# Kernel optimization log

Measured on AMD Instinct MI355X. Metric: run time of the kernel, lower is better.

## Reference

```python
import jax, jax.numpy as jnp
from jax import lax
import numpy as np

NEG = -1e10  # matches the -10000000000.0 boundary in the torch code


def _nw_forward(theta, A):
    """Needleman-Wunsch DP with softmax (logsumexp) smoothed max.

    V[i, j] = theta[i-1, j-1] + LSE(A + V[i-1, j], V[i-1, j-1], A + V[i, j-1])
    with V[0, 0] = 0 and V[i, 0] = V[0, j] = -1e10 otherwise.
    Vectorized over anti-diagonals (wavefront): diag d holds V[i, d-i].
    """
    N, M = theta.shape
    i_idx = jnp.arange(N + 1)

    # diag d=0: only V[0,0]=0 is on it; diag d=1: V[0,1]=V[1,0]=NEG
    d0 = jnp.full((N + 1,), NEG, dtype=theta.dtype).at[0].set(0.0)
    d1 = jnp.full((N + 1,), NEG, dtype=theta.dtype)

    def step(carry, d):
        pprev, prev = carry  # diagonals d-2 and d-1, indexed by i
        j = d - i_idx
        valid = (i_idx >= 1) & (j >= 1) & (j <= M)
        pad = jnp.full((1,), NEG, dtype=theta.dtype)
        up = jnp.concatenate([pad, prev[:-1]])     # V[i-1, j]   (diag d-1, idx i-1)
        diag = jnp.concatenate([pad, pprev[:-1]])  # V[i-1, j-1] (diag d-2, idx i-1)
        left = prev                                # V[i, j-1]   (diag d-1, idx i)
        ic = jnp.clip(i_idx - 1, 0, N - 1)
        jc = jnp.clip(j - 1, 0, M - 1)
        th = jnp.where(valid, theta[ic, jc], 0.0)
        # candidates in original order (x, m, y)
        cand = jnp.stack([A + up, diag, A + left], axis=-1)  # (N+1, 3)
        v = th + jax.nn.logsumexp(cand, axis=-1)
        new = jnp.where(valid, v, NEG)
        return (prev, new), None

    ds = jnp.arange(2, N + M + 1)
    (_, last), _ = lax.scan(step, (d0, d1), ds)
    return last[N]  # V[N, M] lives on diagonal d = N + M at index i = N


def setup_inputs() -> dict:
    key = jax.random.key(0)
    N, M = 2048, 2048
    theta = jax.random.normal(key, (N, M), dtype=jnp.float32)
    A = jnp.asarray(-4.0, dtype=jnp.float32)  # scalar gap penalty
    return {"theta": theta, "A": A}


def reference(theta, A):
    return _nw_forward(theta, A)
```

## Files before the change

kernel.cpp:

```cpp
#include <hip/hip_runtime.h>


constexpr int NDP = 2048;
constexpr int MDP = 2048;
constexpr int G    = 16;
constexpr int RPW  = 128;
constexpr int BATCH = 32;
constexpr int NB    = 68;
constexpr int DTOT  = NDP + MDP;
constexpr int DVB   = 4224;
constexpr float LOG2E = 1.44269504088896340736f;
constexpr float LN2   = 0.69314718055994530942f;

__device__ __forceinline__ float neginf() { return __int_as_float(0xff800000); }

__device__ __forceinline__ void ic_store(float* p, float v) {
  asm volatile("global_store_dword %0, %1, off sc0 sc1" :: "v"(p), "v"(v));
}
__device__ __forceinline__ void ic_store_flag(int* p, int v) {
  asm volatile("s_waitcnt vmcnt(0)\n\tglobal_store_dword %0, %1, off sc0 sc1"
               :: "v"(p), "v"(v));
}
__device__ __forceinline__ float ic_load(const float* p) {
  float r;
  asm volatile("global_load_dword %0, %1, off sc0 sc1\n\ts_waitcnt vmcnt(0)"
               : "=v"(r) : "v"(p));
  return r;
}
__device__ __forceinline__ int ic_load_flag(const int* p) {
  int r;
  asm volatile("global_load_dword %0, %1, off sc0 sc1\n\ts_waitcnt vmcnt(0)"
               : "=v"(r) : "v"(p) : "memory");
  return r;
}

__global__ __launch_bounds__(64)
void nw_pipe(const float* __restrict__ theta, const float* __restrict__ Aptr,
             float* __restrict__ out, float* __restrict__ vbBase,
             int* __restrict__ flags)
{
  const int wg   = blockIdx.x;
  const int lane = threadIdx.x;

  const float A  = Aptr[0];
  const float eA = __builtin_exp2f(A * LOG2E);

  const int S   = wg * RPW + 2;
  const int rA0 = wg * RPW + 2 * lane;
  const int rB0 = rA0 + 1;
  const float* thA_p = theta + (size_t)rA0 * MDP;
  const float* thB_p = theta + (size_t)rB0 * MDP;
  const int endA = rA0 + 1 + MDP;
  const int endB = endA + 1;

  float* vbMine = vbBase + (size_t)wg * DVB;
  const float* vbProd = vbBase + (size_t)(wg - 1) * DVB;
  int* flagProd = flags + (wg - 1) * 16;
  int* flagMine = flags + wg * 16;
  const int eMaxProd = (wg > 0) ? (wg * RPW + MDP) : -1;

  float WA1 = 0.f, WA2 = 0.f, WB1 = 0.f;
  float upPrev = 0.f;
  float bu = 0.f, bd = (wg == 0) ? 1.f : 0.f;
  float oaccF = 0.f;
  bool  init  = (wg == 0);
  float corner = 0.f;
  float vbReg = neginf();

  float tba[4][8], tbb[4][8];
#pragma unroll
  for (int u = 0; u < 4; ++u)
#pragma unroll
    for (int k = 0; k < 8; ++k) {
      int d  = S + 8 * u + k;
      int cA = min(max(d - (rA0 + 1) - 1, 0), MDP - 1);
      int cB = min(max(d - (rB0 + 1) - 1, 0), MDP - 1);
      tba[u][k] = thA_p[cA];
      tbb[u][k] = thB_p[cB];
    }

  if (wg > 0) {
    const int E0 = S - 1;
    const int need = min(E0 + 31, eMaxProd);
    while (ic_load_flag(flagProd) < need) __builtin_amdgcn_s_sleep(1);
    int e  = E0 + (lane & 31);
    int eL = min(max(e, 0), eMaxProd);
    float v0 = ic_load(vbProd + eL);
    vbReg = (e <= eMaxProd) ? v0 : neginf();
    float m = vbReg;
#pragma unroll
    for (int sh = 1; sh < 64; sh <<= 1) m = fmaxf(m, __shfl_xor(m, sh, 64));
    if (m > -1e30f) { oaccF = m; init = true; }
    bu = __builtin_exp2f(fminf(__shfl(vbReg, 0, 64) - oaccF, 120.f));
  }

  for (int b = 0; b < NB; ++b) {
    const int dBase = S + BATCH * b;
#pragma unroll
    for (int u = 0; u < 4; ++u) {
#pragma unroll
      for (int k = 0; k < 8; ++k) {
        const int d = dBase + 8 * u + k;
        float upA = __shfl_up(WB1, 1, 64);
        if (lane == 0) upA = bu;
        float dgA = (lane == 0) ? bd : upPrev;
        const float tA = __builtin_exp2f(tba[u][k] * LOG2E);
        const float tB = __builtin_exp2f(tbb[u][k] * LOG2E);
        float nA = tA * (eA * (upA + WA1) + dgA);
        float nB = tB * (eA * (WA1 + WB1) + WA2);
        nA = (d <= endA) ? nA : 0.f;
        nB = (d <= endB) ? nB : 0.f;
        WA2 = WA1; WA1 = nA; WB1 = nB; upPrev = upA;
        if (lane == 63) {
          float vlog = __builtin_log2f(WB1) + oaccF;
          ic_store(vbMine + d, vlog);
          if (d == DTOT) corner = vlog;
        }
        bd = bu;
        if (!(u == 3 && k == 7)) {
          float v = __shfl(vbReg, 8 * u + k + 1, 64);
          bu = __builtin_exp2f(fminf(v - oaccF, 120.f));
        }
      }
      {
        float m = fmaxf(fmaxf(WA1, WB1), fmaxf(WA2, upPrev));
        m = fmaxf(m, fmaxf(bu, bd));
#pragma unroll
        for (int sh = 1; sh < 64; sh <<= 1) m = fmaxf(m, __shfl_xor(m, sh, 64));
        int e = 0;
        if (m > 0.f) e = (int)((__float_as_uint(m) >> 23) & 0xFFu) - 126;
        if (e != 0) {
          WA1 = ldexpf(WA1, -e); WA2 = ldexpf(WA2, -e); WB1 = ldexpf(WB1, -e);
          upPrev = ldexpf(upPrev, -e);
          bu = ldexpf(bu, -e); bd = ldexpf(bd, -e);
          oaccF += (float)e;
        }
      }
      if (b + 1 < NB) {
#pragma unroll
        for (int k = 0; k < 8; ++k) {
          int d  = dBase + BATCH + 8 * u + k;
          int cA = min(max(d - (rA0 + 1) - 1, 0), MDP - 1);
          int cB = min(max(d - (rB0 + 1) - 1, 0), MDP - 1);
          tba[u][k] = thA_p[cA];
          tbb[u][k] = thB_p[cB];
        }
      }
    }
    if (wg < G - 1 && lane == 63)
      ic_store_flag(flagMine, dBase + BATCH - 1);
    if (b + 1 < NB && wg > 0) {
      const int E0 = S - 1 + BATCH * (b + 1);
      if (E0 <= eMaxProd) {
        const int need = min(E0 + 31, eMaxProd);
        while (ic_load_flag(flagProd) < need) __builtin_amdgcn_s_sleep(1);
        int e  = E0 + (lane & 31);
        int eL = min(max(e, 0), eMaxProd);
        float v0 = ic_load(vbProd + eL);
        vbReg = (e <= eMaxProd) ? v0 : neginf();
      } else {
        vbReg = neginf();
      }
      if (!init) {
        float m = vbReg;
#pragma unroll
        for (int sh = 1; sh < 64; sh <<= 1) m = fmaxf(m, __shfl_xor(m, sh, 64));
        if (m > -1e30f) { oaccF = m; init = true; }
      }
      bu = __builtin_exp2f(fminf(__shfl(vbReg, 0, 64) - oaccF, 120.f));
    }
  }

  if (wg == G - 1 && lane == 63) out[0] = corner * LN2;
}

constexpr int NTH = 512;
constexpr int RPT = 4;
constexpr int NWAVE = NTH / 64;

__global__ __launch_bounds__(NTH)
void nw_single(const float* __restrict__ th, const float* __restrict__ Aptr,
               float* __restrict__ out)
{
  const int tid  = threadIdx.x;
  const int lane = tid & 63;
  const int wid  = tid >> 6;
  __shared__ float handW[2][NTH];
  __shared__ float wmax[2][NWAVE];
  const float A  = Aptr[0];
  const float eA = __builtin_exp2f(A * LOG2E);
  const int i_base = tid * RPT + 1;
  float W10=0.f,W11=0.f,W12=0.f,W13=0.f,W20=0.f,W21=0.f,W22=0.f,W23=0.f;
  float nb1 = 0.f, nb2 = (tid == 0) ? 1.f : 0.f;
  int oacc = 0;
  const float* thb = th + (size_t)(i_base - 1) * MDP;
  auto loadTh = [&](int d) -> float4 {
    float4 r;
    int c0 = min(max(d - i_base - 1, 0), MDP - 1);
    int c1 = min(max(d - i_base - 2, 0), MDP - 1);
    int c2 = min(max(d - i_base - 3, 0), MDP - 1);
    int c3 = min(max(d - i_base - 4, 0), MDP - 1);
    r.x = thb[c0]; r.y = thb[(size_t)MDP + c1];
    r.z = thb[(size_t)2 * MDP + c2]; r.w = thb[(size_t)3 * MDP + c3];
    return r;
  };
  float4 thA = loadTh(2), thB = loadTh(3);
  for (int d = 2; d <= DTOT; ++d) {
    float4 thC = loadTh(d + 2);
    float n0 = __builtin_exp2f(thA.x*LOG2E)*(eA*(nb1+W10)+nb2);
    float n1 = __builtin_exp2f(thA.y*LOG2E)*(eA*(W10+W11)+W20);
    float n2 = __builtin_exp2f(thA.z*LOG2E)*(eA*(W11+W12)+W21);
    float n3 = __builtin_exp2f(thA.w*LOG2E)*(eA*(W12+W13)+W22);
    W20=W10;W21=W11;W22=W12;W23=W13;
    int cb = d - i_base - 1;
    W10 = ((unsigned)(cb)     < (unsigned)MDP) ? n0 : 0.f;
    W11 = ((unsigned)(cb - 1) < (unsigned)MDP) ? n1 : 0.f;
    W12 = ((unsigned)(cb - 2) < (unsigned)MDP) ? n2 : 0.f;
    W13 = ((unsigned)(cb - 3) < (unsigned)MDP) ? n3 : 0.f;
    const int buf = d & 1;
    const bool rs = ((d & 1) == 0);
    const int wbuf = (d >> 1) & 1;
    if (rs) {
      float m = fmaxf(fmaxf(W10,W11),fmaxf(W12,W13));
#pragma unroll
      for (int sh = 1; sh < 64; sh <<= 1) m = fmaxf(m, __shfl_xor(m, sh, 64));
      if (lane == 0) wmax[wbuf][wid] = m;
    }
    handW[buf][tid] = W13;
    __syncthreads();
    nb2 = nb1;
    nb1 = (tid == 0) ? 0.f : handW[buf][tid - 1];
    if (rs) {
      float bm = wmax[wbuf][0];
#pragma unroll
      for (int w = 1; w < NWAVE; ++w) bm = fmaxf(bm, wmax[wbuf][w]);
      int e = 0;
      if (bm > 0.f) e = (int)((__float_as_uint(bm) >> 23) & 0xFFu) - 126;
      if (e != 0) {
        W10=ldexpf(W10,-e);W11=ldexpf(W11,-e);W12=ldexpf(W12,-e);W13=ldexpf(W13,-e);
        W20=ldexpf(W20,-e);W21=ldexpf(W21,-e);W22=ldexpf(W22,-e);W23=ldexpf(W23,-e);
        nb1=ldexpf(nb1,-e);nb2=ldexpf(nb2,-e);
        oacc += e;
      }
    }
    thA = thB; thB = thC;
  }
  if (tid == NTH - 1) out[0] = logf(W13) + (float)oacc * LN2;
}

extern "C" void kernel_launch(void* const* d_in, const int* in_sizes, int n_in,
                              void* d_out, int out_size, void* d_ws, size_t ws_size,
                              hipStream_t stream)
{
  const float* theta = (const float*)d_in[0];
  const float* A     = (const float*)d_in[1];
  float* out = (float*)d_out;

  const size_t need = (size_t)G * DVB * sizeof(float) + G * 16 * sizeof(int);
  if (ws_size >= need) {
    float* vb  = (float*)d_ws;
    int* flags = (int*)((char*)d_ws + (size_t)G * DVB * sizeof(float));
    hipLaunchKernelGGL(nw_pipe, dim3(G), dim3(64), 0, stream, theta, A, out, vb, flags);
  } else {
    hipLaunchKernelGGL(nw_single, dim3(1), dim3(NTH), 0, stream, theta, A, out);
  }
}
```

Measured before the change: 1.154 ms.

## Prefetch theta via async global-to-LDS loads and batch boundary stores

```diff
diff --git a/kernel.cpp b/kernel.cpp
--- a/kernel.cpp
+++ b/kernel.cpp
@@ -34,13 +34,16 @@
   return r;
 }
 
-__global__ __launch_bounds__(64)
+__global__ __launch_bounds__(64, 1)
 void nw_pipe(const float* __restrict__ theta, const float* __restrict__ Aptr,
              float* __restrict__ out, float* __restrict__ vbBase,
              int* __restrict__ flags)
 {
   const int wg   = blockIdx.x;
   const int lane = threadIdx.x;
+
+  __shared__ float ldsT[2][2][BATCH][64];
+  __shared__ float ldsB[BATCH];
 
   const float A  = Aptr[0];
   const float eA = __builtin_exp2f(A * LOG2E);
@@ -59,6 +62,21 @@
   int* flagMine = flags + wg * 16;
   const int eMaxProd = (wg > 0) ? (wg * RPW + MDP) : -1;
 
+  auto stage8 = [&](int tb, int u, int dNext) {
+#pragma unroll
+    for (int h = 0; h < 8; ++h) {
+      const int s2 = 8 * u + h;
+      const int cA = min(max(dNext + s2 - rA0 - 2, 0), MDP - 1);
+      const int cB = min(max(dNext + s2 - rB0 - 2, 0), MDP - 1);
+      __builtin_amdgcn_global_load_lds(
+          (const __attribute__((address_space(1))) void*)(thA_p + cA),
+          (__attribute__((address_space(3))) void*)&ldsT[tb][0][s2][0], 4, 0, 0);
+      __builtin_amdgcn_global_load_lds(
+          (const __attribute__((address_space(1))) void*)(thB_p + cB),
+          (__attribute__((address_space(3))) void*)&ldsT[tb][1][s2][0], 4, 0, 0);
+    }
+  };
+
   float WA1 = 0.f, WA2 = 0.f, WB1 = 0.f;
   float upPrev = 0.f;
   float bu = 0.f, bd = (wg == 0) ? 1.f : 0.f;
@@ -66,18 +84,10 @@
   bool  init  = (wg == 0);
   float corner = 0.f;
   float vbReg = neginf();
-
-  float tba[4][8], tbb[4][8];
-#pragma unroll
-  for (int u = 0; u < 4; ++u)
-#pragma unroll
-    for (int k = 0; k < 8; ++k) {
-      int d  = S + 8 * u + k;
-      int cA = min(max(d - (rA0 + 1) - 1, 0), MDP - 1);
-      int cB = min(max(d - (rB0 + 1) - 1, 0), MDP - 1);
-      tba[u][k] = thA_p[cA];
-      tbb[u][k] = thB_p[cB];
-    }
+  int   buf = 0;
+
+#pragma unroll
+  for (int u = 0; u < 4; ++u) stage8(0, u, S);
 
   if (wg > 0) {
     const int E0 = S - 1;
@@ -93,19 +103,25 @@
     if (m > -1e30f) { oaccF = m; init = true; }
     bu = __builtin_exp2f(fminf(__shfl(vbReg, 0, 64) - oaccF, 120.f));
   }
+  asm volatile("s_waitcnt vmcnt(0)" ::: "memory");
+  __builtin_amdgcn_sched_barrier(0);
 
   for (int b = 0; b < NB; ++b) {
     const int dBase = S + BATCH * b;
 #pragma unroll
     for (int u = 0; u < 4; ++u) {
+      if (b + 1 < NB) stage8(buf ^ 1, u, dBase + BATCH);
 #pragma unroll
       for (int k = 0; k < 8; ++k) {
-        const int d = dBase + 8 * u + k;
+        const int s = 8 * u + k;
+        const int d = dBase + s;
+        const float thAv = ldsT[buf][0][s][lane];
+        const float thBv = ldsT[buf][1][s][lane];
         float upA = __shfl_up(WB1, 1, 64);
         if (lane == 0) upA = bu;
         float dgA = (lane == 0) ? bd : upPrev;
-        const float tA = __builtin_exp2f(tba[u][k] * LOG2E);
-        const float tB = __builtin_exp2f(tbb[u][k] * LOG2E);
+        const float tA = __builtin_exp2f(thAv * LOG2E);
+        const float tB = __builtin_exp2f(thBv * LOG2E);
         float nA = tA * (eA * (upA + WA1) + dgA);
         float nB = tB * (eA * (WA1 + WB1) + WA2);
         nA = (d <= endA) ? nA : 0.f;
@@ -113,12 +129,12 @@
         WA2 = WA1; WA1 = nA; WB1 = nB; upPrev = upA;
         if (lane == 63) {
           float vlog = __builtin_log2f(WB1) + oaccF;
-          ic_store(vbMine + d, vlog);
+          ldsB[s] = vlog;
           if (d == DTOT) corner = vlog;
         }
         bd = bu;
         if (!(u == 3 && k == 7)) {
-          float v = __shfl(vbReg, 8 * u + k + 1, 64);
+          float v = __shfl(vbReg, s + 1, 64);
           bu = __builtin_exp2f(fminf(v - oaccF, 120.f));
         }
       }
@@ -136,16 +152,10 @@
           oaccF += (float)e;
         }
       }
-      if (b + 1 < NB) {
-#pragma unroll
-        for (int k = 0; k < 8; ++k) {
-          int d  = dBase + BATCH + 8 * u + k;
-          int cA = min(max(d - (rA0 + 1) - 1, 0), MDP - 1);
-          int cB = min(max(d - (rB0 + 1) - 1, 0), MDP - 1);
-          tba[u][k] = thA_p[cA];
-          tbb[u][k] = thB_p[cB];
-        }
-      }
+    }
+    if (lane < 32) {
+      float v = ldsB[lane];
+      ic_store(vbMine + dBase + lane, v);
     }
     if (wg < G - 1 && lane == 63)
       ic_store_flag(flagMine, dBase + BATCH - 1);
@@ -169,6 +179,9 @@
       }
       bu = __builtin_exp2f(fminf(__shfl(vbReg, 0, 64) - oaccF, 120.f));
     }
+    asm volatile("s_waitcnt vmcnt(0)" ::: "memory");
+    __builtin_amdgcn_sched_barrier(0);
+    buf ^= 1;
   }
 
   if (wg == G - 1 && lane == 63) out[0] = corner * LN2;
```

Result: slower. 1.357 ms (+17.6%).
